# Kernel optimization log

Hardware: AMD Instinct MI355X
Metric: run time of the kernel (lower is better)

The kernel has to match this reference:

```python
import jax, jax.numpy as jnp
import numpy as np

B, S, E = 2, 2048, 2048
H = 16              # num value heads
D = E // H // 2     # = 64, half head dim (Q/K head dim)
LAMBDA_INIT = 0.8 - 0.6 * float(np.exp(-0.3 * 12))
NORM_EPS = 1e-5


def setup_inputs() -> dict:
    key = jax.random.key(0)
    ks = jax.random.split(key, 10)
    std = 0.02
    x = jax.random.normal(ks[0], (B, S, E), jnp.float32)
    Wq = jax.random.normal(ks[1], (E, E), jnp.float32) * std
    Wk = jax.random.normal(ks[2], (E, E), jnp.float32) * std
    Wv = jax.random.normal(ks[3], (E, E), jnp.float32) * std
    Wo = jax.random.normal(ks[4], (E, E), jnp.float32) * std
    lambda_q1 = jax.random.normal(ks[5], (D,), jnp.float32) * 0.1
    lambda_q2 = jax.random.normal(ks[6], (D,), jnp.float32) * 0.1
    lambda_k1 = jax.random.normal(ks[7], (D,), jnp.float32) * 0.1
    lambda_k2 = jax.random.normal(ks[8], (D,), jnp.float32) * 0.1
    norm_w = jnp.ones((2 * D,), jnp.float32)
    # standard RoPE angle table: (S, D//2)
    inv_freq = 1.0 / (10000.0 ** (np.arange(0, D, 2, dtype=np.float32) / D))
    ang = np.outer(np.arange(S, dtype=np.float32), inv_freq)
    freqs_cos = jnp.asarray(np.cos(ang), jnp.float32)
    freqs_sin = jnp.asarray(np.sin(ang), jnp.float32)
    return {"x": x, "Wq": Wq, "Wk": Wk, "Wv": Wv, "Wo": Wo,
            "lambda_q1": lambda_q1, "lambda_q2": lambda_q2,
            "lambda_k1": lambda_k1, "lambda_k2": lambda_k2,
            "norm_w": norm_w, "freqs_cos": freqs_cos, "freqs_sin": freqs_sin,
            "start_pos": 0}


def _rope(t, cos, sin):
    # t: (B, S, nh, D); complex rotation over pairs along last dim
    tr = t.reshape(*t.shape[:-1], -1, 2)
    tre, tim = tr[..., 0], tr[..., 1]
    c = cos[None, :, None, :]
    s = sin[None, :, None, :]
    out_re = tre * c - tim * s
    out_im = tre * s + tim * c
    return jnp.stack([out_re, out_im], axis=-1).reshape(t.shape)


def reference(x, Wq, Wk, Wv, Wo, lambda_q1, lambda_q2, lambda_k1, lambda_k2,
              norm_w, freqs_cos, freqs_sin, start_pos):
    bsz, tgt_len, _ = x.shape
    scaling = D ** (-0.5)
    q = (x @ Wq.T).reshape(bsz, tgt_len, 2 * H, D)
    k = (x @ Wk.T).reshape(bsz, tgt_len, 2 * H, D)
    v = (x @ Wv.T).reshape(bsz, tgt_len, H, 2 * D)
    q = _rope(q, freqs_cos, freqs_sin)
    k = _rope(k, freqs_cos, freqs_sin)
    q = (q * scaling).transpose(0, 2, 1, 3)      # (B, 2H, S, D)
    keys = k.transpose(0, 2, 1, 3)               # (B, 2H, S, D)
    values = v.transpose(0, 2, 1, 3)             # (B, H, S, 2D)
    scores = jnp.einsum('bhsd,bhtd->bhst', q, keys)
    causal = jnp.where(jnp.arange(tgt_len)[None, :] > jnp.arange(tgt_len)[:, None],
                       jnp.float32(-jnp.inf), jnp.float32(0.0))
    scores = scores + causal
    attn = jax.nn.softmax(scores.astype(jnp.float32), axis=-1)
    lam1 = jnp.exp(jnp.sum(lambda_q1 * lambda_k1))
    lam2 = jnp.exp(jnp.sum(lambda_q2 * lambda_k2))
    lambda_full = lam1 - lam2 + LAMBDA_INIT
    attn = attn.reshape(bsz, H, 2, tgt_len, tgt_len)
    attn_diff = attn[:, :, 0] - lambda_full * attn[:, :, 1]   # (B, H, S, S)
    ctx = jnp.einsum('bhst,bhtd->bhsd', attn_diff, values)    # (B, H, S, 2D)
    # per-head RMSNorm over 2D channel dim
    ctx = ctx * jax.lax.rsqrt(jnp.mean(ctx * ctx, axis=-1, keepdims=True) + NORM_EPS)
    ctx = ctx * norm_w
    ctx = ctx.transpose(0, 2, 1, 3).reshape(bsz, tgt_len, H * 2 * D)
    return ctx @ Wo.T
```

## Files before the change

### kernel.cpp

```cpp
#include <hip/hip_runtime.h>
#include <hip/hip_bf16.h>
#include <stdint.h>

typedef __hip_bfloat16 bf16;
typedef __attribute__((ext_vector_type(8))) short short8;
typedef __attribute__((ext_vector_type(4))) short s4v;
typedef __attribute__((ext_vector_type(4))) float floatx4;

#define MFMA16(a, b, c) __builtin_amdgcn_mfma_f32_16x16x32_bf16((a), (b), (c), 0, 0, 0)
#define LAMBDA_INIT_F 0.7836057665f

__device__ __forceinline__ void async16(const void* g, void* l) {
    __builtin_amdgcn_global_load_lds(
        (const __attribute__((address_space(1))) void*)g,
        (__attribute__((address_space(3))) void*)(uintptr_t)l,
        16, 0, 0);
}

__device__ __forceinline__ float loadf(const void* p, size_t idx, int isbf) {
    if (isbf) return __bfloat162float(((const bf16*)p)[idx]);
    return ((const float*)p)[idx];
}

__global__ void detect_dtype(const unsigned short* __restrict__ x, int* __restrict__ flag) {
    const int t = threadIdx.x;
    const unsigned short u = x[2 * t];
    const int e = (u >> 7) & 0xFF;
    int sane = (e >= 110 && e <= 130) ? 1 : 0;
#pragma unroll
    for (int m = 32; m > 0; m >>= 1) sane += __shfl_xor(sane, m);
    if (t == 0) flag[0] = (sane >= 32) ? 1 : 0;
}

__global__ __launch_bounds__(256) void to_bf16(const void* __restrict__ src,
                                               bf16* __restrict__ dst, int n,
                                               const int* __restrict__ flag) {
    const int i = (blockIdx.x * 256 + threadIdx.x) * 8;
    if (i >= n) return;
    if (flag[0]) {
        *(short8*)(dst + i) = *(const short8*)((const bf16*)src + i);
    } else {
        const float* f = (const float*)src + i;
        short8 r;
#pragma unroll
        for (int j = 0; j < 8; ++j) {
            bf16 h = __float2bfloat16(f[j]);
            r[j] = __builtin_bit_cast(short, h);
        }
        *(short8*)(dst + i) = r;
    }
}

__global__ __launch_bounds__(256) void gemm_bt_ep(const bf16* __restrict__ A,
                                                  const bf16* __restrict__ B,
                                                  void* __restrict__ C,
                                                  int M, int N, int K,
                                                  const int* __restrict__ flag,
                                                  const void* __restrict__ fcos,
                                                  const void* __restrict__ fsin,
                                                  int mode) {
    __shared__ __align__(16) bf16 As[128 * 32];
    __shared__ __align__(16) bf16 Bs[128 * 32];

    const int tid  = threadIdx.x;
    const int lane = tid & 63;
    const int quad = lane >> 4;
    const int l16  = lane & 15;
    const int w    = tid >> 6;
    const int wr   = w >> 1, wc = w & 1;
    const int bm   = blockIdx.y, bn = blockIdx.x;

    floatx4 acc[4][4];
#pragma unroll
    for (int i = 0; i < 4; ++i)
#pragma unroll
        for (int j = 0; j < 4; ++j)
#pragma unroll
            for (int r = 0; r < 4; ++r) acc[i][j][r] = 0.0f;

    for (int k0 = 0; k0 < K; k0 += 32) {
        __syncthreads();
#pragma unroll
        for (int i = 0; i < 2; ++i) {
            const int c     = i * 256 + tid;
            const int row   = c >> 2;
            const int inner = c & 3;
            async16(A + (size_t)(bm * 128 + row) * K + k0 + inner * 8, (char*)As + c * 16);
            async16(B + (size_t)(bn * 128 + row) * K + k0 + inner * 8, (char*)Bs + c * 16);
        }
        __syncthreads();

        short8 af[4], bfr[4];
#pragma unroll
        for (int i = 0; i < 4; ++i)
            af[i] = *(const short8*)((const char*)As + (wr * 64 + i * 16 + l16) * 64 + quad * 16);
#pragma unroll
        for (int j = 0; j < 4; ++j)
            bfr[j] = *(const short8*)((const char*)Bs + (wc * 64 + j * 16 + l16) * 64 + quad * 16);
#pragma unroll
        for (int i = 0; i < 4; ++i)
#pragma unroll
            for (int j = 0; j < 4; ++j)
                acc[i][j] = MFMA16(af[i], bfr[j], acc[i][j]);
    }

    const int isbf = flag[0];
    if (mode == 3) {
#pragma unroll
        for (int i = 0; i < 4; ++i)
#pragma unroll
            for (int j = 0; j < 4; ++j) {
                const int n  = bn * 128 + wc * 64 + j * 16 + l16;
                const int m0 = bm * 128 + wr * 64 + i * 16 + quad * 4;
                const int bb = m0 >> 11;
                const int s0 = m0 & 2047;
                s4v pk;
#pragma unroll
                for (int r = 0; r < 4; ++r) {
                    bf16 hv = __float2bfloat16(acc[i][j][r]);
                    pk[r] = __builtin_bit_cast(short, hv);
                }
                *(s4v*)((bf16*)C + ((size_t)(bb * 2048 + n)) * 2048 + s0) = pk;
            }
    } else if (mode == 1 || mode == 2) {
        const float qs = (mode == 1) ? 0.125f : 1.0f;
#pragma unroll
        for (int i = 0; i < 4; ++i)
#pragma unroll
            for (int j = 0; j < 4; ++j) {
                const int n   = bn * 128 + wc * 64 + j * 16 + l16;
                const int jp  = (n & 63) >> 1;
                const float sg = (n & 1) ? 1.0f : -1.0f;
#pragma unroll
                for (int r = 0; r < 4; ++r) {
                    const int m = bm * 128 + wr * 64 + i * 16 + quad * 4 + r;
                    const int s = m & 2047;
                    const float v  = acc[i][j][r];
                    const float pv = __shfl_xor(v, 1);
                    const float ct = loadf(fcos, (size_t)s * 32 + jp, isbf);
                    const float st = loadf(fsin, (size_t)s * 32 + jp, isbf);
                    const float out = (v * ct + sg * pv * st) * qs;
                    ((bf16*)C)[(size_t)m * N + n] = __float2bfloat16(out);
                }
            }
    } else {
        const int c_bf = (mode == 4) ? isbf : 1;
#pragma unroll
        for (int i = 0; i < 4; ++i)
#pragma unroll
            for (int j = 0; j < 4; ++j) {
                const int n = bn * 128 + wc * 64 + j * 16 + l16;
#pragma unroll
                for (int r = 0; r < 4; ++r) {
                    const int m = bm * 128 + wr * 64 + i * 16 + quad * 4 + r;
                    if (c_bf) ((bf16*)C)[(size_t)m * N + n] = __float2bfloat16(acc[i][j][r]);
                    else      ((float*)C)[(size_t)m * N + n] = acc[i][j][r];
                }
            }
    }
}

__global__ void lambda_kernel(const void* lq1, const void* lq2,
                              const void* lk1, const void* lk2,
                              float* out, const int* __restrict__ flag) {
    const int isbf = flag[0];
    const int t = threadIdx.x;
    float p1 = loadf(lq1, t, isbf) * loadf(lk1, t, isbf);
    float p2 = loadf(lq2, t, isbf) * loadf(lk2, t, isbf);
#pragma unroll
    for (int m = 32; m > 0; m >>= 1) {
        p1 += __shfl_xor(p1, m);
        p2 += __shfl_xor(p2, m);
    }
    if (t == 0) out[0] = expf(p1) - expf(p2) + LAMBDA_INIT_F;
}

__global__ __launch_bounds__(256) void diff_attn(const bf16* __restrict__ Q,
                                                 const bf16* __restrict__ K,
                                                 const bf16* __restrict__ Vt,
                                                 bf16* __restrict__ ctx,
                                                 const float* __restrict__ lam,
                                                 const void* __restrict__ norm_w,
                                                 const int* __restrict__ flag) {
    __shared__ __align__(16) char smem[55296];
    bf16* K1s = (bf16*)smem;
    bf16* K2s = (bf16*)(smem + 8192);
    bf16* Vs  = (bf16*)(smem + 16384);
    char* pool = smem + 32768;

    const int isbf = flag[0];
    const int tid  = threadIdx.x;
    const int lane = tid & 63;
    const int quad = lane >> 4;
    const int l16  = lane & 15;
    const int w    = tid >> 6;
    const int t7   = l16 & 7;

    const int bidx = blockIdx.x;
    const int c8   = bidx & 7;
    const int r6   = bidx >> 3;
    const int p    = r6 & 15;
    const int grp  = (r6 >> 4) * 8 + c8;
    const int h    = grp & 15;
    const int b    = grp >> 4;

    const float lambda_full = lam[0];
    float nw[8];
#pragma unroll
    for (int j = 0; j < 8; ++j) nw[j] = loadf(norm_w, j * 16 + l16, isbf);

    bf16* P1s = (bf16*)(pool + w * 2816);
    bf16* P2s = (bf16*)(pool + 11264 + w * 2816);

    for (int tsel = 0; tsel < 2; ++tsel) {
        const int qt = tsel ? (31 - p) : p;
        const int q0 = qt * 64;

        __syncthreads();

#pragma unroll
        for (int i = 0; i < 2; ++i) {
            const int c = i * 256 + tid;
            const int row = c >> 3, cc = c & 7;
            const int inner = cc ^ (row & 7);
            async16(Q + ((size_t)(b * 2048 + q0 + row) * 32 + 2 * h) * 64 + inner * 8,
                    pool + c * 16);
            async16(Q + ((size_t)(b * 2048 + q0 + row) * 32 + 2 * h + 1) * 64 + inner * 8,
                    pool + 8192 + c * 16);
        }
        __syncthreads();

        short8 qf1[2], qf2[2];
        {
            const int rho = w * 16 + l16;
#pragma unroll
            for (int c = 0; c < 2; ++c) {
                const int ch = (c * 4 + quad) ^ t7;
                qf1[c] = *(const short8*)(pool + rho * 128 + ch * 16);
                qf2[c] = *(const short8*)(pool + 8192 + rho * 128 + ch * 16);
            }
        }

        floatx4 O1[8], O2[8];
#pragma unroll
        for (int j = 0; j < 8; ++j)
#pragma unroll
            for (int r = 0; r < 4; ++r) { O1[j][r] = 0.0f; O2[j][r] = 0.0f; }
        float lp1[4] = {0.f, 0.f, 0.f, 0.f};
        float lp2[4] = {0.f, 0.f, 0.f, 0.f};

        for (int kt0 = 0; kt0 <= q0; kt0 += 64) {
            __syncthreads();
#pragma unroll
            for (int i = 0; i < 2; ++i) {
                const int c = i * 256 + tid;
                const int row = c >> 3, cc = c & 7;
                const int inner = cc ^ (row & 7);
                async16(K + ((size_t)(b * 2048 + kt0 + row) * 32 + 2 * h) * 64 + inner * 8,
                        (char*)K1s + c * 16);
                async16(K + ((size_t)(b * 2048 + kt0 + row) * 32 + 2 * h + 1) * 64 + inner * 8,
                        (char*)K2s + c * 16);
            }
#pragma unroll
            for (int i = 0; i < 4; ++i) {
                const int c = i * 256 + tid;
                const int d = c >> 3, cc = c & 7;
                const int inner = cc ^ (d & 7);
                async16(Vt + ((size_t)(b * 16 + h) * 128 + d) * 2048 + kt0 + inner * 8,
                        (char*)Vs + c * 16);
            }
            __syncthreads();

            floatx4 s1[4], s2[4];
#pragma unroll
            for (int j = 0; j < 4; ++j)
#pragma unroll
                for (int r = 0; r < 4; ++r) { s1[j][r] = 0.0f; s2[j][r] = 0.0f; }
#pragma unroll
            for (int c = 0; c < 2; ++c) {
                const int ch = ((c * 4 + quad) ^ t7) * 16;
#pragma unroll
                for (int j = 0; j < 4; ++j) {
                    short8 k1f = *(const short8*)((const char*)K1s + (j * 16 + l16) * 128 + ch);
                    s1[j] = MFMA16(qf1[c], k1f, s1[j]);
                    short8 k2f = *(const short8*)((const char*)K2s + (j * 16 + l16) * 128 + ch);
                    s2[j] = MFMA16(qf2[c], k2f, s2[j]);
                }
            }

            if (kt0 == q0) {
#pragma unroll
                for (int j = 0; j < 4; ++j)
#pragma unroll
                    for (int r = 0; r < 4; ++r)
                        if (j * 16 + l16 > w * 16 + quad * 4 + r) {
                            s1[j][r] = -1e30f;
                            s2[j][r] = -1e30f;
                        }
            }

#pragma unroll
            for (int j = 0; j < 4; ++j)
#pragma unroll
                for (int r = 0; r < 4; ++r) {
                    const float e1 = __expf(s1[j][r]);
                    const float e2 = __expf(s2[j][r]);
                    lp1[r] += e1;
                    lp2[r] += e2;
                    P1s[(quad * 4 + r) * 88 + j * 16 + l16] = __float2bfloat16(e1);
                    P2s[(quad * 4 + r) * 88 + j * 16 + l16] = __float2bfloat16(e2);
                }

#pragma unroll
            for (int c = 0; c < 2; ++c) {
                short8 a1 = *(const short8*)((const char*)P1s + l16 * 176 + c * 64 + quad * 16);
                short8 a2 = *(const short8*)((const char*)P2s + l16 * 176 + c * 64 + quad * 16);
                const int ch = ((c * 4 + quad) ^ t7) * 16;
#pragma unroll
                for (int j = 0; j < 8; ++j) {
                    short8 vb = *(const short8*)((const char*)Vs + (j * 16 + l16) * 128 + ch);
                    O1[j] = MFMA16(a1, vb, O1[j]);
                    O2[j] = MFMA16(a2, vb, O2[j]);
                }
            }
        }

#pragma unroll
        for (int r = 0; r < 4; ++r) {
            float t1 = lp1[r], t2 = lp2[r];
            t1 += __shfl_xor(t1, 1); t2 += __shfl_xor(t2, 1);
            t1 += __shfl_xor(t1, 2); t2 += __shfl_xor(t2, 2);
            t1 += __shfl_xor(t1, 4); t2 += __shfl_xor(t2, 4);
            t1 += __shfl_xor(t1, 8); t2 += __shfl_xor(t2, 8);
            const float i1 = 1.0f / t1;
            const float i2 = lambda_full / t2;
            float cv[8];
            float ss = 0.0f;
#pragma unroll
            for (int j = 0; j < 8; ++j) {
                const float v = O1[j][r] * i1 - O2[j][r] * i2;
                cv[j] = v;
                ss += v * v;
            }
            ss += __shfl_xor(ss, 1);
            ss += __shfl_xor(ss, 2);
            ss += __shfl_xor(ss, 4);
            ss += __shfl_xor(ss, 8);
            const float scale = rsqrtf(ss * (1.0f / 128.0f) + 1e-5f);
            const int row = q0 + w * 16 + quad * 4 + r;
            const size_t base = ((size_t)(b * 2048) + row) * 2048 + h * 128;
#pragma unroll
            for (int j = 0; j < 8; ++j)
                ctx[base + j * 16 + l16] = __float2bfloat16(cv[j] * scale * nw[j]);
        }
    }
}

extern "C" void kernel_launch(void* const* d_in, const int* in_sizes, int n_in,
                              void* d_out, int out_size, void* d_ws, size_t ws_size,
                              hipStream_t stream) {
    const void* x   = d_in[0];
    const void* Wq  = d_in[1];
    const void* Wk  = d_in[2];
    const void* Wv  = d_in[3];
    const void* Wo  = d_in[4];
    const void* lq1 = d_in[5];
    const void* lq2 = d_in[6];
    const void* lk1 = d_in[7];
    const void* lk2 = d_in[8];
    const void* nw  = d_in[9];
    const void* fc  = d_in[10];
    const void* fs  = d_in[11];

    const size_t BUF = (size_t)4096 * 2048 * sizeof(bf16);
    if (ws_size < 4 * BUF + 64) return;
    char* ws = (char*)d_ws;
    bf16*  qbuf  = (bf16*)(ws);
    bf16*  kbuf  = (bf16*)(ws + BUF);
    bf16*  vbuf  = (bf16*)(ws + 2 * BUF);
    bf16*  vtbuf = (bf16*)(ws + 3 * BUF);
    float* lamb  = (float*)(ws + 4 * BUF);
    int*   flag  = (int*)(ws + 4 * BUF + 8);
    bf16*  xb    = vbuf;
    bf16*  wslot = (bf16*)d_out;
    bf16*  ctxb  = vbuf;

    const int NX = 2 * 2048 * 2048;
    const int NW = 2048 * 2048;

    detect_dtype<<<1, 64, 0, stream>>>((const unsigned short*)x, flag);
    to_bf16<<<NX / 2048, 256, 0, stream>>>(x, xb, NX, flag);

    dim3 gg(16, 32);
    to_bf16<<<NW / 2048, 256, 0, stream>>>(Wq, wslot, NW, flag);
    gemm_bt_ep<<<gg, 256, 0, stream>>>(xb, wslot, qbuf, 4096, 2048, 2048, flag, fc, fs, 1);
    to_bf16<<<NW / 2048, 256, 0, stream>>>(Wk, wslot, NW, flag);
    gemm_bt_ep<<<gg, 256, 0, stream>>>(xb, wslot, kbuf, 4096, 2048, 2048, flag, fc, fs, 2);
    to_bf16<<<NW / 2048, 256, 0, stream>>>(Wv, wslot, NW, flag);
    gemm_bt_ep<<<gg, 256, 0, stream>>>(xb, wslot, vtbuf, 4096, 2048, 2048, flag, fc, fs, 3);

    lambda_kernel<<<1, 64, 0, stream>>>(lq1, lq2, lk1, lk2, lamb, flag);

    diff_attn<<<512, 256, 0, stream>>>(qbuf, kbuf, vtbuf, ctxb, lamb, nw, flag);

    to_bf16<<<NW / 2048, 256, 0, stream>>>(Wo, qbuf, NW, flag);
    gemm_bt_ep<<<gg, 256, 0, stream>>>(ctxb, qbuf, d_out, 4096, 2048, 2048, flag, fc, fs, 4);
}
```

Measured before the change: 542.9 us.

## Fuse Q/K/V projections into one GEMM launch and skip bf16 weight copies

New measurement: 501.2 us. 1.08x faster.

```diff
diff --git a/kernel.cpp b/kernel.cpp
--- a/kernel.cpp
+++ b/kernel.cpp
@@ -34,7 +34,9 @@
 
 __global__ __launch_bounds__(256) void to_bf16(const void* __restrict__ src,
                                                bf16* __restrict__ dst, int n,
-                                               const int* __restrict__ flag) {
+                                               const int* __restrict__ flag,
+                                               int skip_if_bf16) {
+    if (skip_if_bf16 && flag[0]) return;
     const int i = (blockIdx.x * 256 + threadIdx.x) * 8;
     if (i >= n) return;
     if (flag[0]) {
@@ -48,6 +50,111 @@
             r[j] = __builtin_bit_cast(short, h);
         }
         *(short8*)(dst + i) = r;
+    }
+}
+
+__device__ __forceinline__ void gemm_core(const bf16* __restrict__ A,
+                                          const bf16* __restrict__ B,
+                                          void* __restrict__ C,
+                                          int N, int K, int bm, int bn,
+                                          const int* __restrict__ flag,
+                                          const void* __restrict__ fcos,
+                                          const void* __restrict__ fsin,
+                                          int mode, bf16* As, bf16* Bs) {
+    const int tid  = threadIdx.x;
+    const int lane = tid & 63;
+    const int quad = lane >> 4;
+    const int l16  = lane & 15;
+    const int w    = tid >> 6;
+    const int wr   = w >> 1, wc = w & 1;
+
+    floatx4 acc[4][4];
+#pragma unroll
+    for (int i = 0; i < 4; ++i)
+#pragma unroll
+        for (int j = 0; j < 4; ++j)
+#pragma unroll
+            for (int r = 0; r < 4; ++r) acc[i][j][r] = 0.0f;
+
+    for (int k0 = 0; k0 < K; k0 += 32) {
+        __syncthreads();
+#pragma unroll
+        for (int i = 0; i < 2; ++i) {
+            const int c     = i * 256 + tid;
+            const int row   = c >> 2;
+            const int inner = c & 3;
+            async16(A + (size_t)(bm * 128 + row) * K + k0 + inner * 8, (char*)As + c * 16);
+            async16(B + (size_t)(bn * 128 + row) * K + k0 + inner * 8, (char*)Bs + c * 16);
+        }
+        __syncthreads();
+
+        short8 af[4], bfr[4];
+#pragma unroll
+        for (int i = 0; i < 4; ++i)
+            af[i] = *(const short8*)((const char*)As + (wr * 64 + i * 16 + l16) * 64 + quad * 16);
+#pragma unroll
+        for (int j = 0; j < 4; ++j)
+            bfr[j] = *(const short8*)((const char*)Bs + (wc * 64 + j * 16 + l16) * 64 + quad * 16);
+#pragma unroll
+        for (int i = 0; i < 4; ++i)
+#pragma unroll
+            for (int j = 0; j < 4; ++j)
+                acc[i][j] = MFMA16(af[i], bfr[j], acc[i][j]);
+    }
+
+    const int isbf = flag[0];
+    if (mode == 3) {
+#pragma unroll
+        for (int i = 0; i < 4; ++i)
+#pragma unroll
+            for (int j = 0; j < 4; ++j) {
+                const int n  = bn * 128 + wc * 64 + j * 16 + l16;
+                const int m0 = bm * 128 + wr * 64 + i * 16 + quad * 4;
+                const int bb = m0 >> 11;
+                const int s0 = m0 & 2047;
+                s4v pk;
+#pragma unroll
+                for (int r = 0; r < 4; ++r) {
+                    bf16 hv = __float2bfloat16(acc[i][j][r]);
+                    pk[r] = __builtin_bit_cast(short, hv);
+                }
+                *(s4v*)((bf16*)C + ((size_t)(bb * 2048 + n)) * 2048 + s0) = pk;
+            }
+    } else if (mode == 1 || mode == 2) {
+        const float qs = (mode == 1) ? 0.125f : 1.0f;
+#pragma unroll
+        for (int i = 0; i < 4; ++i)
+#pragma unroll
+            for (int j = 0; j < 4; ++j) {
+                const int n   = bn * 128 + wc * 64 + j * 16 + l16;
+                const int jp  = (n & 63) >> 1;
+                const float sg = (n & 1) ? 1.0f : -1.0f;
+#pragma unroll
+                for (int r = 0; r < 4; ++r) {
+                    const int m = bm * 128 + wr * 64 + i * 16 + quad * 4 + r;
+                    const int s = m & 2047;
+                    const float v  = acc[i][j][r];
+                    const float pv = __shfl_xor(v, 1);
+                    const float ct = loadf(fcos, (size_t)s * 32 + jp, isbf);
+                    const float st = loadf(fsin, (size_t)s * 32 + jp, isbf);
+                    const float out = (v * ct + sg * pv * st) * qs;
+                    ((bf16*)C)[(size_t)m * N + n] = __float2bfloat16(out);
+                }
+            }
+    } else {
+        const int c_bf = (mode == 4) ? isbf : 1;
+#pragma unroll
+        for (int i = 0; i < 4; ++i)
+#pragma unroll
+            for (int j = 0; j < 4; ++j) {
+                const int n = bn * 128 + wc * 64 + j * 16 + l16;
+#pragma unroll
+                for (int r = 0; r < 4; ++r) {
+                    const int m = bm * 128 + wr * 64 + i * 16 + quad * 4 + r;
+                    if (c_bf) ((bf16*)C)[(size_t)m * N + n] = __float2bfloat16(acc[i][j][r]);
+                    else      ((float*)C)[(size_t)m * N + n] = acc[i][j][r];
+                }
+            }
     }
 }
 
@@ -61,103 +168,34 @@
                                                   int mode) {
     __shared__ __align__(16) bf16 As[128 * 32];
     __shared__ __align__(16) bf16 Bs[128 * 32];
-
-    const int tid  = threadIdx.x;
-    const int lane = tid & 63;
-    const int quad = lane >> 4;
-    const int l16  = lane & 15;
-    const int w    = tid >> 6;
-    const int wr   = w >> 1, wc = w & 1;
-    const int bm   = blockIdx.y, bn = blockIdx.x;
-
-    floatx4 acc[4][4];
-#pragma unroll
-    for (int i = 0; i < 4; ++i)
-#pragma unroll
-        for (int j = 0; j < 4; ++j)
-#pragma unroll
-            for (int r = 0; r < 4; ++r) acc[i][j][r] = 0.0f;
-
-    for (int k0 = 0; k0 < K; k0 += 32) {
-        __syncthreads();
-#pragma unroll
-        for (int i = 0; i < 2; ++i) {
-            const int c     = i * 256 + tid;
-            const int row   = c >> 2;
-            const int inner = c & 3;
-            async16(A + (size_t)(bm * 128 + row) * K + k0 + inner * 8, (char*)As + c * 16);
-            async16(B + (size_t)(bn * 128 + row) * K + k0 + inner * 8, (char*)Bs + c * 16);
-        }
-        __syncthreads();
-
-        short8 af[4], bfr[4];
-#pragma unroll
-        for (int i = 0; i < 4; ++i)
-            af[i] = *(const short8*)((const char*)As + (wr * 64 + i * 16 + l16) * 64 + quad * 16);
-#pragma unroll
-        for (int j = 0; j < 4; ++j)
-            bfr[j] = *(const short8*)((const char*)Bs + (wc * 64 + j * 16 + l16) * 64 + quad * 16);
-#pragma unroll
-        for (int i = 0; i < 4; ++i)
-#pragma unroll
-            for (int j = 0; j < 4; ++j)
-                acc[i][j] = MFMA16(af[i], bfr[j], acc[i][j]);
-    }
-
+    gemm_core(A, B, C, N, K, blockIdx.y, blockIdx.x, flag, fcos, fsin, mode, As, Bs);
+}
+
+__global__ __launch_bounds__(256) void gemm_qkv(const bf16* __restrict__ A,
+                                                const bf16* __restrict__ Wq_s,
+                                                const bf16* __restrict__ Wk_s,
+                                                const bf16* __restrict__ Wv_s,
+                                                const void* __restrict__ WqR,
+                                                const void* __restrict__ WkR,
+                                                const void* __restrict__ WvR,
+                                                bf16* __restrict__ qbuf,
+                                                bf16* __restrict__ kbuf,
+                                                bf16* __restrict__ vtbuf,
+                                                int K, const int* __restrict__ flag,
+                                                const void* __restrict__ fcos,
+                                                const void* __restrict__ fsin) {
+    __shared__ __align__(16) bf16 As[128 * 32];
+    __shared__ __align__(16) bf16 Bs[128 * 32];
+    const int wsel = blockIdx.x >> 4;
+    const int bnl  = blockIdx.x & 15;
     const int isbf = flag[0];
-    if (mode == 3) {
-#pragma unroll
-        for (int i = 0; i < 4; ++i)
-#pragma unroll
-            for (int j = 0; j < 4; ++j) {
-                const int n  = bn * 128 + wc * 64 + j * 16 + l16;
-                const int m0 = bm * 128 + wr * 64 + i * 16 + quad * 4;
-                const int bb = m0 >> 11;
-                const int s0 = m0 & 2047;
-                s4v pk;
-#pragma unroll
-                for (int r = 0; r < 4; ++r) {
-                    bf16 hv = __float2bfloat16(acc[i][j][r]);
-                    pk[r] = __builtin_bit_cast(short, hv);
-                }
-                *(s4v*)((bf16*)C + ((size_t)(bb * 2048 + n)) * 2048 + s0) = pk;
-            }
-    } else if (mode == 1 || mode == 2) {
-        const float qs = (mode == 1) ? 0.125f : 1.0f;
-#pragma unroll
-        for (int i = 0; i < 4; ++i)
-#pragma unroll
-            for (int j = 0; j < 4; ++j) {
-                const int n   = bn * 128 + wc * 64 + j * 16 + l16;
-                const int jp  = (n & 63) >> 1;
-                const float sg = (n & 1) ? 1.0f : -1.0f;
-#pragma unroll
-                for (int r = 0; r < 4; ++r) {
-                    const int m = bm * 128 + wr * 64 + i * 16 + quad * 4 + r;
-                    const int s = m & 2047;
-                    const float v  = acc[i][j][r];
-                    const float pv = __shfl_xor(v, 1);
-                    const float ct = loadf(fcos, (size_t)s * 32 + jp, isbf);
-                    const float st = loadf(fsin, (size_t)s * 32 + jp, isbf);
-                    const float out = (v * ct + sg * pv * st) * qs;
-                    ((bf16*)C)[(size_t)m * N + n] = __float2bfloat16(out);
-                }
-            }
-    } else {
-        const int c_bf = (mode == 4) ? isbf : 1;
-#pragma unroll
-        for (int i = 0; i < 4; ++i)
-#pragma unroll
-            for (int j = 0; j < 4; ++j) {
-                const int n = bn * 128 + wc * 64 + j * 16 + l16;
-#pragma unroll
-                for (int r = 0; r < 4; ++r) {
-                    const int m = bm * 128 + wr * 64 + i * 16 + quad * 4 + r;
-                    if (c_bf) ((bf16*)C)[(size_t)m * N + n] = __float2bfloat16(acc[i][j][r]);
-                    else      ((float*)C)[(size_t)m * N + n] = acc[i][j][r];
-                }
-            }
-    }
+    const bf16* Bp;
+    void* Cp;
+    int mode;
+    if (wsel == 0)      { Bp = isbf ? (const bf16*)WqR : Wq_s; Cp = qbuf;  mode = 1; }
+    else if (wsel == 1) { Bp = isbf ? (const bf16*)WkR : Wk_s; Cp = kbuf;  mode = 2; }
+    else                { Bp = isbf ? (const bf16*)WvR : Wv_s; Cp = vtbuf; mode = 3; }
+    gemm_core(A, Bp, Cp, 2048, K, blockIdx.y, bnl, flag, fcos, fsin, mode, As, Bs);
 }
 
 __global__ void lambda_kernel(const void* lq1, const void* lq2,
@@ -382,27 +420,31 @@
     float* lamb  = (float*)(ws + 4 * BUF);
     int*   flag  = (int*)(ws + 4 * BUF + 8);
     bf16*  xb    = vbuf;
-    bf16*  wslot = (bf16*)d_out;
     bf16*  ctxb  = vbuf;
+
+    bf16* wq_s = (bf16*)d_out;
+    bf16* wk_s = wq_s + (size_t)2048 * 2048;
+    bf16* wv_s = wk_s + (size_t)2048 * 2048;
 
     const int NX = 2 * 2048 * 2048;
     const int NW = 2048 * 2048;
 
     detect_dtype<<<1, 64, 0, stream>>>((const unsigned short*)x, flag);
-    to_bf16<<<NX / 2048, 256, 0, stream>>>(x, xb, NX, flag);
-
+    to_bf16<<<NX / 2048, 256, 0, stream>>>(x, xb, NX, flag, 0);
+
+    to_bf16<<<NW / 2048, 256, 0, stream>>>(Wq, wq_s, NW, flag, 1);
+    to_bf16<<<NW / 2048, 256, 0, stream>>>(Wk, wk_s, NW, flag, 1);
+    to_bf16<<<NW / 2048, 256, 0, stream>>>(Wv, wv_s, NW, flag, 1);
+
+    dim3 gq(48, 32);
+    gemm_qkv<<<gq, 256, 0, stream>>>(xb, wq_s, wk_s, wv_s, Wq, Wk, Wv,
+                                     qbuf, kbuf, vtbuf, 2048, flag, fc, fs);
+
+    lambda_kernel<<<1, 64, 0, stream>>>(lq1, lq2, lk1, lk2, lamb, flag);
+
+    diff_attn<<<512, 256, 0, stream>>>(qbuf, kbuf, vtbuf, ctxb, lamb, nw, flag);
+
+    to_bf16<<<NW / 2048, 256, 0, stream>>>(Wo, qbuf, NW, flag, 0);
     dim3 gg(16, 32);
-    to_bf16<<<NW / 2048, 256, 0, stream>>>(Wq, wslot, NW, flag);
-    gemm_bt_ep<<<gg, 256, 0, stream>>>(xb, wslot, qbuf, 4096, 2048, 2048, flag, fc, fs, 1);
-    to_bf16<<<NW / 2048, 256, 0, stream>>>(Wk, wslot, NW, flag);
-    gemm_bt_ep<<<gg, 256, 0, stream>>>(xb, wslot, kbuf, 4096, 2048, 2048, flag, fc, fs, 2);
-    to_bf16<<<NW / 2048, 256, 0, stream>>>(Wv, wslot, NW, flag);
-    gemm_bt_ep<<<gg, 256, 0, stream>>>(xb, wslot, vtbuf, 4096, 2048, 2048, flag, fc, fs, 3);
-
-    lambda_kernel<<<1, 64, 0, stream>>>(lq1, lq2, lk1, lk2, lamb, flag);
-
-    diff_attn<<<512, 256, 0, stream>>>(qbuf, kbuf, vtbuf, ctxb, lamb, nw, flag);
-
-    to_bf16<<<NW / 2048, 256, 0, stream>>>(Wo, qbuf, NW, flag);
     gemm_bt_ep<<<gg, 256, 0, stream>>>(ctxb, qbuf, d_out, 4096, 2048, 2048, flag, fc, fs, 4);
 }
```
